# Kernel tuning notes

Hardware: AMD Instinct MI355X
Metric: run time of the kernel (lower is better)

The kernel has to match this reference:

```python
import jax, jax.numpy as jnp
import numpy as np

B, V, T, CIN, WEMB, H, NW = 32, 500, 24, 2, 4, 64, 8
C0 = CIN + WEMB  # 6 channels entering first layer


def _stglstm(x, supports, Wg, bg, Wo, bo, out_len=None, final_layer=False):
    # x: (B, C, V, T); supports: (S, V, V)
    Bb, C, Vv, Tt = x.shape
    T_steps = out_len if out_len is not None else Tt
    if final_layer:
        xs = jnp.broadcast_to(x[:, :, :, -1][None], (T_steps, Bb, C, Vv))
    else:
        xs = jnp.moveaxis(x, 3, 0)  # (T, B, C, V)

    def step(carry, xt):
        hx, cx = carry
        comb = xt + hx  # (B, C, V)
        feats = [comb]
        for s in range(supports.shape[0]):  # fixed small support_len loop
            x1 = jnp.einsum('bcv,vw->bcw', comb, supports[s])
            x2 = jnp.einsum('bcv,vw->bcw', x1, supports[s])
            feats += [x1, x2]  # order-2 diffusion
        g = jnp.concatenate(feats, axis=1)  # (B, 7C, V)
        gates = jnp.einsum('bgv,og->bov', g, Wg) + bg[None, :, None]  # (B, 4C, V)
        i, f, cg, o = jnp.split(gates, 4, axis=1)
        cy = jax.nn.sigmoid(f) * cx + jax.nn.sigmoid(i) * cg  # cellgate is linear (no tanh), as in source
        hy = jax.nn.sigmoid(o) * jnp.tanh(cy)
        return (hy, cy), hy

    h0 = jnp.zeros((Bb, C, Vv), x.dtype)
    _, hs = jax.lax.scan(step, (h0, h0), xs)  # hs: (T, B, C, V)
    hs = jnp.moveaxis(hs, 0, 3)  # (B, C, V, T)
    return jnp.einsum('bcvt,oc->bovt', hs, Wo) + bo[None, :, None, None]


def _se(x, Wa, Wb):
    y = x.mean(axis=(2, 3))  # (B, C) global avg pool
    y = jax.nn.sigmoid(jax.nn.relu(y @ Wa.T) @ Wb.T)
    return x * y[:, :, None, None]


def setup_inputs():
    key = jax.random.key(0)
    ks = jax.random.split(key, 24)

    def n(k, shape, s=0.05):
        return jax.random.normal(k, shape, jnp.float32) * s

    A = jax.random.uniform(ks[0], (3, V, V), jnp.float32)
    A = A / A.sum(-1, keepdims=True)  # row-stochastic random-walk matrices
    return {
        'x': n(ks[1], (B, CIN, V, T), 1.0),
        'supports': A,
        'w_type': jax.random.randint(ks[2], (B, V, T), 0, NW, dtype=jnp.int32),
        'Wemb': n(ks[3], (NW, WEMB)),
        'Wg0': n(ks[4], (4 * C0, 7 * C0)), 'bg0': jnp.zeros((4 * C0,), jnp.float32),
        'Wo0': n(ks[5], (H, C0)), 'bo0': jnp.zeros((H,), jnp.float32),
        'Ws0a': n(ks[6], (H // 16, H)), 'Ws0b': n(ks[7], (H, H // 16)),
        'Wg1': n(ks[8], (4 * H, 7 * H)), 'bg1': jnp.zeros((4 * H,), jnp.float32),
        'Wo1': n(ks[9], (H, H)), 'bo1': jnp.zeros((H,), jnp.float32),
        'Ws1a': n(ks[10], (H // 16, H)), 'Ws1b': n(ks[11], (H, H // 16)),
        'Wg2': n(ks[12], (4 * H, 7 * H)), 'bg2': jnp.zeros((4 * H,), jnp.float32),
        'Wo2': n(ks[13], (H, H)), 'bo2': jnp.zeros((H,), jnp.float32),
        'Wg3': n(ks[14], (4 * H, 7 * H)), 'bg3': jnp.zeros((4 * H,), jnp.float32),
        'Wo3': n(ks[15], (2, H)), 'bo3': jnp.zeros((2,), jnp.float32),
    }


def reference(x, supports, w_type, Wemb, Wg0, bg0, Wo0, bo0, Ws0a, Ws0b,
              Wg1, bg1, Wo1, bo1, Ws1a, Ws1b, Wg2, bg2, Wo2, bo2,
              Wg3, bg3, Wo3, bo3):
    w_vec = Wemb[w_type]  # (B, V, T, wemb)
    w_vec = jnp.transpose(w_vec, (0, 3, 1, 2))  # (B, wemb, V, T)
    h = jnp.concatenate([x, w_vec], axis=1)  # (B, CIN+wemb, V, T)
    h = _stglstm(h, supports, Wg0, bg0, Wo0, bo0)
    h = _se(h, Ws0a, Ws0b)
    h = _stglstm(h, supports, Wg1, bg1, Wo1, bo1)
    h = _se(h, Ws1a, Ws1b)
    h = _stglstm(h, supports, Wg2, bg2, Wo2, bo2)
    out = _stglstm(h, supports, Wg3, bg3, Wo3, bo3, out_len=T, final_layer=True)
    return out  # (B, 2, V, out_len)
```

## Files before the change

kernel.cpp:

```cpp
#include <hip/hip_runtime.h>
#include <math.h>

#define NV 500
#define NB 32
#define NT 24
#define NH 64

typedef _Float16 f16;
typedef _Float16 f16x8 __attribute__((ext_vector_type(8)));
typedef _Float16 f16x4 __attribute__((ext_vector_type(4)));
typedef float    f32x4 __attribute__((ext_vector_type(4)));

__device__ __forceinline__ float sigm(float x){ return 1.f/(1.f+expf(-x)); }

__global__ void k_a2(const float* __restrict__ A, float* __restrict__ A2)
{
    int idx = blockIdx.x*256 + threadIdx.x;
    if (idx >= 3*500*500) return;
    int wv = idx % 500; int rest = idx/500; int r = rest % 500; int s = rest/500;
    const float* Ar = A + ((size_t)s*500 + r)*500;
    const float* Ac = A + (size_t)s*500*500 + wv;
    float a = 0.f;
    for (int u = 0; u < 500; u++) a += Ar[u]*Ac[(size_t)u*500];
    A2[idx] = a;
}

__global__ void k_acat(const float* __restrict__ A, const float* __restrict__ A2,
                       f16* __restrict__ AcatT)
{
    int idx = blockIdx.x*256 + threadIdx.x;
    if (idx >= 3072*512) return;
    int k = idx & 511;
    int n = idx >> 9;
    int j = n >> 9, wv = n & 511;
    float val = 0.f;
    if (k < 500 && wv < 500) {
        int s = j >> 1;
        const float* M = (j & 1) ? A2 : A;
        val = M[((size_t)s*500 + k)*500 + wv];
    }
    AcatT[idx] = (f16)val;
}

__global__ void k_f2h(const float* __restrict__ src, f16* __restrict__ dst, int n)
{
    int idx = blockIdx.x*256 + threadIdx.x;
    if (idx < n) dst[idx] = (f16)src[idx];
}

__global__ __launch_bounds__(256)
void k_diff(const f16* __restrict__ Acv, const f16* __restrict__ Bt,
            f16* __restrict__ fout, int Mtot, int C, int G)
{
    __shared__ f16 lA[128*32];
    __shared__ f16 lB[128*32];
    const int tid = threadIdx.x;
    const int n0 = blockIdx.x*128, m0 = blockIdx.y*128;
    const int r0 = tid>>2, c0 = tid&3;
    const int swz0 = r0*32 + ((c0 ^ ((r0>>1)&3))<<3);
    const int swz1 = swz0 + 64*32;
    int mA0 = m0 + r0;      if (mA0 > Mtot-1) mA0 = Mtot-1;
    int mA1 = m0 + r0 + 64; if (mA1 > Mtot-1) mA1 = Mtot-1;
    const f16* gA0 = Acv + (size_t)mA0*512 + c0*8;
    const f16* gA1 = Acv + (size_t)mA1*512 + c0*8;
    const f16* gB0 = Bt + (size_t)(n0+r0)*512 + c0*8;
    const f16* gB1 = Bt + (size_t)(n0+r0+64)*512 + c0*8;

    const int w = tid>>6, lane = tid&63;
    const int wr = (w>>1)<<6, wc = (w&1)<<6;
    const int fm = lane&15, fk = lane>>4;
    const int fch = (fk ^ ((fm>>1)&3))<<3;

    f32x4 acc[4][4];
    #pragma unroll
    for (int i=0;i<4;i++)
        #pragma unroll
        for (int j=0;j<4;j++) acc[i][j] = (f32x4){0.f,0.f,0.f,0.f};

    f32x4 ra0 = *(const f32x4*)gA0, ra1 = *(const f32x4*)gA1;
    f32x4 rb0 = *(const f32x4*)gB0, rb1 = *(const f32x4*)gB1;

    for (int ks = 0; ks < 16; ks++) {
        __syncthreads();
        *(f32x4*)(lA + swz0) = ra0;  *(f32x4*)(lA + swz1) = ra1;
        *(f32x4*)(lB + swz0) = rb0;  *(f32x4*)(lB + swz1) = rb1;
        if (ks < 15) {
            int o = (ks+1)*32;
            ra0 = *(const f32x4*)(gA0 + o); ra1 = *(const f32x4*)(gA1 + o);
            rb0 = *(const f32x4*)(gB0 + o); rb1 = *(const f32x4*)(gB1 + o);
        }
        __syncthreads();
        f16x8 af[4], bf[4];
        #pragma unroll
        for (int i=0;i<4;i++) af[i] = *(const f16x8*)(lA + (wr + i*16 + fm)*32 + fch);
        #pragma unroll
        for (int j=0;j<4;j++) bf[j] = *(const f16x8*)(lB + (wc + j*16 + fm)*32 + fch);
        #pragma unroll
        for (int i=0;i<4;i++)
            #pragma unroll
            for (int j=0;j<4;j++)
                acc[i][j] = __builtin_amdgcn_mfma_f32_16x16x32_f16(af[i], bf[j], acc[i][j], 0, 0, 0);
    }

    #pragma unroll
    for (int j=0;j<4;j++) {
        int col = n0 + wc + j*16 + fm;
        int jb = col >> 9, wv = col & 511;
        if (wv >= 500) continue;
        #pragma unroll
        for (int i=0;i<4;i++) {
            int mb = m0 + wr + i*16 + fk*4;
            if (C == 64) {
                if (mb >= Mtot) continue;
                int b = mb >> 6, c = mb & 63;
                f16x4 h4;
                h4[0]=(f16)acc[i][j][0]; h4[1]=(f16)acc[i][j][1];
                h4[2]=(f16)acc[i][j][2]; h4[3]=(f16)acc[i][j][3];
                *(f16x4*)(fout + ((size_t)b*512 + wv)*G + C + jb*C + c) = h4;
            } else {
                #pragma unroll
                for (int r=0;r<4;r++) {
                    int m = mb + r;
                    if (m < Mtot) {
                        int b = m / C, c = m - b*C;
                        fout[((size_t)b*512 + wv)*G + C + jb*C + c] = (f16)acc[i][j][r];
                    }
                }
            }
        }
    }
}

__global__ __launch_bounds__(256)
void k_gates(const f16* __restrict__ fT, const f16* __restrict__ Wg,
             const float* __restrict__ bg, float* __restrict__ gT)
{
    __shared__ f16 lA[128*32];
    __shared__ f16 lB[128*32];
    const int tid = threadIdx.x;
    const int n0 = blockIdx.x*128, m0 = blockIdx.y*128, b = blockIdx.z;
    const f16* Ab = fT + (size_t)b*512*448;
    const int r0 = tid>>2, c0 = tid&3;
    const int swz0 = r0*32 + ((c0 ^ ((r0>>1)&3))<<3);
    const int swz1 = swz0 + 64*32;
    const f16* gA0 = Ab + (size_t)(m0+r0)*448 + c0*8;
    const f16* gA1 = Ab + (size_t)(m0+r0+64)*448 + c0*8;
    const f16* gB0 = Wg + (size_t)(n0+r0)*448 + c0*8;
    const f16* gB1 = Wg + (size_t)(n0+r0+64)*448 + c0*8;

    const int w = tid>>6, lane = tid&63;
    const int wr = (w>>1)<<6, wc = (w&1)<<6;
    const int fm = lane&15, fk = lane>>4;
    const int fch = (fk ^ ((fm>>1)&3))<<3;

    f32x4 acc[4][4];
    #pragma unroll
    for (int i=0;i<4;i++)
        #pragma unroll
        for (int j=0;j<4;j++) acc[i][j] = (f32x4){0.f,0.f,0.f,0.f};

    f32x4 ra0 = *(const f32x4*)gA0, ra1 = *(const f32x4*)gA1;
    f32x4 rb0 = *(const f32x4*)gB0, rb1 = *(const f32x4*)gB1;

    for (int ks = 0; ks < 14; ks++) {
        __syncthreads();
        *(f32x4*)(lA + swz0) = ra0;  *(f32x4*)(lA + swz1) = ra1;
        *(f32x4*)(lB + swz0) = rb0;  *(f32x4*)(lB + swz1) = rb1;
        if (ks < 13) {
            int o = (ks+1)*32;
            ra0 = *(const f32x4*)(gA0 + o); ra1 = *(const f32x4*)(gA1 + o);
            rb0 = *(const f32x4*)(gB0 + o); rb1 = *(const f32x4*)(gB1 + o);
        }
        __syncthreads();
        f16x8 af[4], bf[4];
        #pragma unroll
        for (int i=0;i<4;i++) af[i] = *(const f16x8*)(lA + (wr + i*16 + fm)*32 + fch);
        #pragma unroll
        for (int j=0;j<4;j++) bf[j] = *(const f16x8*)(lB + (wc + j*16 + fm)*32 + fch);
        #pragma unroll
        for (int i=0;i<4;i++)
            #pragma unroll
            for (int j=0;j<4;j++)
                acc[i][j] = __builtin_amdgcn_mfma_f32_16x16x32_f16(af[i], bf[j], acc[i][j], 0, 0, 0);
    }

    #pragma unroll
    for (int j=0;j<4;j++) {
        int o = n0 + wc + j*16 + fm;
        float bias = bg[o];
        #pragma unroll
        for (int i=0;i<4;i++) {
            int vb = m0 + wr + i*16 + fk*4;
            #pragma unroll
            for (int r=0;r<4;r++) {
                int v = vb + r;
                if (v < 500)
                    gT[((size_t)b*512 + v)*256 + o] = acc[i][j][r] + bias;
            }
        }
    }
}

__global__ __launch_bounds__(256)
void k_comb(const void* __restrict__ src, int srcF16, int Cin,
            const float* __restrict__ Wo, const float* __restrict__ bo,
            const float* __restrict__ se, const f16* __restrict__ hprev,
            f16* __restrict__ fT, f16* __restrict__ ccv)
{
    __shared__ float WoS[64*64];
    __shared__ float seS[64], boS[64];
    __shared__ f16 combS[64*72];
    int b = blockIdx.y, v0 = blockIdx.x*64;
    int tid = threadIdx.x;
    if (Cin > 0) {
        for (int i = tid; i < 64*Cin; i += 256) WoS[i] = Wo[i];
        if (tid < 64) { boS[tid] = bo[tid]; seS[tid] = se ? se[b*64+tid] : 1.f; }
    }
    __syncthreads();
    int vloc = tid>>2, part = tid&3;
    int v = v0 + vloc;
    float val[16];
    if (Cin == 0) {
        const float* x3 = (const float*)src + ((size_t)b*512 + v)*64 + part*16;
        #pragma unroll
        for (int k=0;k<16;k++) val[k] = x3[k];
    } else {
        float acc[16];
        #pragma unroll
        for (int k=0;k<16;k++) acc[k] = 0.f;
        if (srcF16) {
            const f16* sp = (const f16*)src + ((size_t)b*512 + v)*64;
            for (int cc=0; cc<Cin; cc++) {
                float xv = (float)sp[cc];
                #pragma unroll
                for (int k=0;k<16;k++) acc[k] += WoS[(part*16+k)*Cin + cc]*xv;
            }
        } else {
            const float* sp = (const float*)src + ((size_t)b*512 + v)*(size_t)Cin;
            for (int cc=0; cc<Cin; cc++) {
                float xv = sp[cc];
                #pragma unroll
                for (int k=0;k<16;k++) acc[k] += WoS[(part*16+k)*Cin + cc]*xv;
            }
        }
        #pragma unroll
        for (int k=0;k<16;k++) { int c = part*16+k; val[k] = seS[c]*(acc[k] + boS[c]); }
    }
    if (hprev) {
        const f16* hp = hprev + ((size_t)b*512 + v)*64 + part*16;
        #pragma unroll
        for (int k=0;k<16;k++) val[k] += (float)hp[k];
    }
    if (v >= 500) {
        #pragma unroll
        for (int k=0;k<16;k++) val[k] = 0.f;
    }
    #pragma unroll
    for (int k=0;k<16;k++) combS[vloc*72 + part*16 + k] = (f16)val[k];
    __syncthreads();
    {
        int vl = tid>>2, p = tid&3;
        f32x4 d0 = *(f32x4*)(combS + vl*72 + p*16);
        f32x4 d1 = *(f32x4*)(combS + vl*72 + p*16 + 8);
        f16* dst = fT + ((size_t)b*512 + (v0+vl))*448 + p*16;
        *(f32x4*)dst = d0; *(f32x4*)(dst+8) = d1;
    }
    {
        int c = tid>>2, p = tid&3;
        alignas(16) f16 tmp[16];
        #pragma unroll
        for (int k=0;k<16;k++) tmp[k] = combS[(p*16+k)*72 + c];
        f16* dst = ccv + ((size_t)b*64 + c)*512 + v0 + p*16;
        *(f32x4*)dst = *(f32x4*)tmp; *(f32x4*)(dst+8) = *(f32x4*)(tmp+8);
    }
}

__global__ void k_lstm(const float* __restrict__ gT, float* __restrict__ cst,
                       f16* __restrict__ hdst, int first)
{
    int id = blockIdx.x*4 + (threadIdx.x>>6);
    if (id >= NB*500) return;
    int b = id / 500, v = id - b*500;
    int c = threadIdx.x & 63;
    const float* g = gT + ((size_t)b*512 + v)*256;
    float gi = g[c], gf = g[64+c], gc = g[128+c], go = g[192+c];
    size_t ci = ((size_t)b*512 + v)*64 + c;
    float cx = first ? 0.f : cst[ci];
    float cy = sigm(gf)*cx + sigm(gi)*gc;
    cst[ci] = cy;
    hdst[ci] = (f16)(sigm(go)*tanhf(cy));
}

__global__ void k_lstm3out(const float* __restrict__ gT, float* __restrict__ cst,
                           f16* __restrict__ hdst, const float* __restrict__ Wo3,
                           const float* __restrict__ bo3, float* __restrict__ out,
                           int t, int first)
{
    int id = blockIdx.x*4 + (threadIdx.x>>6);
    if (id >= NB*500) return;
    int b = id / 500, v = id - b*500;
    int c = threadIdx.x & 63;
    const float* g = gT + ((size_t)b*512 + v)*256;
    float gi = g[c], gf = g[64+c], gc = g[128+c], go = g[192+c];
    size_t ci = ((size_t)b*512 + v)*64 + c;
    float cx = first ? 0.f : cst[ci];
    float cy = sigm(gf)*cx + sigm(gi)*gc;
    cst[ci] = cy;
    float hy = sigm(go)*tanhf(cy);
    hdst[ci] = (f16)hy;
    float r0 = Wo3[c]*hy, r1 = Wo3[64+c]*hy;
    #pragma unroll
    for (int s = 32; s > 0; s >>= 1) {
        r0 += __shfl_down(r0, s, 64);
        r1 += __shfl_down(r1, s, 64);
    }
    if (c == 0) {
        out[((size_t)(b*2+0)*500 + v)*24 + t] = r0 + bo3[0];
        out[((size_t)(b*2+1)*500 + v)*24 + t] = r1 + bo3[1];
    }
}

__global__ void k_comb0(const float* __restrict__ x, const int* __restrict__ wt,
                        const float* __restrict__ Wemb, const float* __restrict__ hs0T,
                        f16* __restrict__ f0T, f16* __restrict__ ccv0, int t)
{
    int b = blockIdx.y;
    int v = blockIdx.x*256 + threadIdx.x;
    if (v >= 512) return;
    if (v >= 500) {
        #pragma unroll
        for (int c=0;c<6;c++) ccv0[((size_t)b*6 + c)*512 + v] = (f16)0.f;
        return;
    }
    float vals[6];
    vals[0] = x[((size_t)(b*2+0)*500 + v)*24 + t];
    vals[1] = x[((size_t)(b*2+1)*500 + v)*24 + t];
    int wty = wt[((size_t)b*500 + v)*24 + t];
    vals[2] = Wemb[wty*4+0]; vals[3] = Wemb[wty*4+1];
    vals[4] = Wemb[wty*4+2]; vals[5] = Wemb[wty*4+3];
    if (t > 0) {
        const float* hp = hs0T + (((size_t)(t-1)*NB + b)*512 + v)*6;
        #pragma unroll
        for (int c=0;c<6;c++) vals[c] += hp[c];
    }
    #pragma unroll
    for (int c=0;c<6;c++) {
        f16 h = (f16)vals[c];
        f0T[((size_t)b*512 + v)*42 + c] = h;
        ccv0[((size_t)b*6 + c)*512 + v] = h;
    }
}

__global__ void k_gates0(const float* __restrict__ Wg, const float* __restrict__ bgv,
                         const f16* __restrict__ f0T, float* __restrict__ g0T)
{
    __shared__ float WgS[24*42];
    for (int i = threadIdx.x; i < 24*42; i += 256) WgS[i] = Wg[i];
    __syncthreads();
    int idx = blockIdx.x*256 + threadIdx.x;
    if (idx >= NB*24*500) return;
    int v = idx % 500; int rest = idx/500; int o = rest % 24; int b = rest/24;
    const f16* fp = f0T + ((size_t)b*512 + v)*42;
    float a = bgv[o];
    #pragma unroll
    for (int g = 0; g < 42; g++) a += WgS[o*42+g]*(float)fp[g];
    g0T[((size_t)b*512 + v)*24 + o] = a;
}

__global__ void k_lstm0(const float* __restrict__ g0T, float* __restrict__ cst0,
                        float* __restrict__ hs0T, int t)
{
    int idx = blockIdx.x*256 + threadIdx.x;
    if (idx >= NB*500*6) return;
    int c = idx % 6; int rest = idx/6; int v = rest % 500; int b = rest/500;
    const float* g = g0T + ((size_t)b*512 + v)*24;
    float gi = g[c], gf = g[6+c], gc = g[12+c], go = g[18+c];
    size_t ci = ((size_t)b*500 + v)*6 + c;
    float cx = t ? cst0[ci] : 0.f;
    float cy = sigm(gf)*cx + sigm(gi)*gc;
    cst0[ci] = cy;
    hs0T[(((size_t)t*NB + b)*512 + v)*6 + c] = sigm(go)*tanhf(cy);
}

__global__ void k_mean0(const float* __restrict__ hs0T, float* __restrict__ mean0)
{
    int b = blockIdx.x;
    float acc[6] = {0,0,0,0,0,0};
    for (int i = threadIdx.x; i < 24*500; i += 256) {
        int tt = i/500, v = i - tt*500;
        const float* p = hs0T + (((size_t)tt*NB + b)*512 + v)*6;
        #pragma unroll
        for (int c=0;c<6;c++) acc[c] += p[c];
    }
    __shared__ float red[256];
    for (int c=0;c<6;c++) {
        red[threadIdx.x] = acc[c]; __syncthreads();
        for (int s=128;s>0;s>>=1) { if (threadIdx.x<s) red[threadIdx.x]+=red[threadIdx.x+s]; __syncthreads(); }
        if (threadIdx.x==0) mean0[b*6+c] = red[0]/12000.f;
        __syncthreads();
    }
}

__global__ void k_mean1(const f16* __restrict__ hs1T, float* __restrict__ mean1)
{
    int cg = blockIdx.x, b = blockIdx.y;
    float acc[8] = {0,0,0,0,0,0,0,0};
    for (int i = threadIdx.x; i < 24*500; i += 256) {
        int tt = i/500, v = i - tt*500;
        const f16* p = hs1T + (((size_t)tt*NB + b)*512 + v)*64 + cg*8;
        #pragma unroll
        for (int c=0;c<8;c++) acc[c] += (float)p[c];
    }
    __shared__ float red[256];
    for (int c=0;c<8;c++) {
        red[threadIdx.x] = acc[c]; __syncthreads();
        for (int s=128;s>0;s>>=1) { if (threadIdx.x<s) red[threadIdx.x]+=red[threadIdx.x+s]; __syncthreads(); }
        if (threadIdx.x==0) mean1[b*64 + cg*8 + c] = red[0]/12000.f;
        __syncthreads();
    }
}

__global__ void k_se(const float* __restrict__ meanhs, const float* __restrict__ Wo,
                     const float* __restrict__ bo, int Cin,
                     const float* __restrict__ Wa, const float* __restrict__ Wb,
                     float* __restrict__ se)
{
    int b = blockIdx.x; int c = threadIdx.x;
    __shared__ float y[64]; __shared__ float a[4];
    float acc = bo[c];
    for (int j = 0; j < Cin; j++) acc += Wo[(size_t)c*Cin + j] * meanhs[b*Cin + j];
    y[c] = acc;
    __syncthreads();
    if (c < 4) {
        float s = 0.f;
        for (int j = 0; j < 64; j++) s += Wa[c*64 + j] * y[j];
        a[c] = fmaxf(s, 0.f);
    }
    __syncthreads();
    float s = 0.f;
    #pragma unroll
    for (int j = 0; j < 4; j++) s += Wb[c*4 + j] * a[j];
    se[b*64 + c] = 1.f/(1.f + expf(-s));
}

__global__ void k_x3(const f16* __restrict__ h, const float* __restrict__ Wo,
                     const float* __restrict__ bo, float* __restrict__ x3T)
{
    int idx = blockIdx.x*256 + threadIdx.x;
    if (idx >= NB*500*64) return;
    int c = idx & 63; int rest = idx >> 6; int v = rest % 500; int b = rest/500;
    const f16* hp = h + ((size_t)b*512 + v)*64;
    float a = bo[c];
    #pragma unroll 8
    for (int cc = 0; cc < 64; cc++) a += Wo[c*64 + cc]*(float)hp[cc];
    x3T[((size_t)b*512 + v)*64 + c] = a;
}

extern "C" void kernel_launch(void* const* d_in, const int* in_sizes, int n_in,
                              void* d_out, int out_size, void* d_ws, size_t ws_size,
                              hipStream_t stream)
{
    const float* x    = (const float*)d_in[0];
    const float* sup  = (const float*)d_in[1];
    const int*   wt   = (const int*)  d_in[2];
    const float* Wemb = (const float*)d_in[3];
    const float* Wg0  = (const float*)d_in[4];
    const float* bg0  = (const float*)d_in[5];
    const float* Wo0  = (const float*)d_in[6];
    const float* bo0  = (const float*)d_in[7];
    const float* Wa0  = (const float*)d_in[8];
    const float* Wb0  = (const float*)d_in[9];
    const float* Wg1  = (const float*)d_in[10];
    const float* bg1  = (const float*)d_in[11];
    const float* Wo1  = (const float*)d_in[12];
    const float* bo1  = (const float*)d_in[13];
    const float* Wa1  = (const float*)d_in[14];
    const float* Wb1  = (const float*)d_in[15];
    const float* Wg2  = (const float*)d_in[16];
    const float* bg2  = (const float*)d_in[17];
    const float* Wo2  = (const float*)d_in[18];
    const float* bo2  = (const float*)d_in[19];
    const float* Wg3  = (const float*)d_in[20];
    const float* bg3  = (const float*)d_in[21];
    const float* Wo3  = (const float*)d_in[22];
    const float* bo3  = (const float*)d_in[23];
    float* out = (float*)d_out;
    (void)in_sizes; (void)n_in; (void)out_size; (void)ws_size;

    char* ws = (char*)d_ws;
    size_t off = 0;
    f16*   AcatT  = (f16*)(ws + off);   off += (size_t)3072*512*2;
    float* A2     = (float*)(ws + off); off += (size_t)3*500*500*4;
    f16*   WgF1   = (f16*)(ws + off);   off += (size_t)256*448*2;
    f16*   WgF2   = (f16*)(ws + off);   off += (size_t)256*448*2;
    f16*   WgF3   = (f16*)(ws + off);   off += (size_t)256*448*2;
    f16*   comb_cv= (f16*)(ws + off);   off += (size_t)2048*512*2;
    f16*   ccv0   = (f16*)(ws + off);   off += (size_t)192*512*2;
    f16*   featsT = (f16*)(ws + off);   off += (size_t)NB*512*448*2;
    f16*   f0T    = (f16*)(ws + off);   off += (size_t)NB*512*42*2;
    float* gatesT = (float*)(ws + off); off += (size_t)NB*512*256*4;
    float* g0T    = (float*)(ws + off); off += (size_t)NB*512*24*4;
    float* hs0T   = (float*)(ws + off); off += (size_t)NT*NB*512*6*4;
    f16*   hs1T   = (f16*)(ws + off);   off += (size_t)NT*NB*512*64*2;
    f16*   hT     = (f16*)(ws + off);   off += (size_t)NB*512*64*2;
    float* cstT   = (float*)(ws + off); off += (size_t)NB*512*64*4;
    float* cst0   = (float*)(ws + off); off += (size_t)NB*500*6*4;
    float* x3T    = (float*)(ws + off); off += (size_t)NB*512*64*4;
    float* mean0  = (float*)(ws + off); off += 8192;
    float* se0    = (float*)(ws + off); off += 8192;
    float* mean1  = (float*)(ws + off); off += 8192;
    float* se1    = (float*)(ws + off); off += 8192;

    const size_t sliceH = (size_t)NB*512*64;
    const size_t slice0 = (size_t)NB*512*6;

    k_a2  <<<(3*500*500 + 255)/256, 256, 0, stream>>>(sup, A2);
    k_acat<<<(3072*512 + 255)/256, 256, 0, stream>>>(sup, A2, AcatT);
    k_f2h <<<(256*448 + 255)/256, 256, 0, stream>>>(Wg1, WgF1, 256*448);
    k_f2h <<<(256*448 + 255)/256, 256, 0, stream>>>(Wg2, WgF2, 256*448);
    k_f2h <<<(256*448 + 255)/256, 256, 0, stream>>>(Wg3, WgF3, 256*448);

    for (int t = 0; t < NT; t++) {
        k_comb0 <<<dim3(2, NB), 256, 0, stream>>>(x, wt, Wemb, hs0T, f0T, ccv0, t);
        k_diff  <<<dim3(24, 2), 256, 0, stream>>>(ccv0, AcatT, f0T, 192, 6, 42);
        k_gates0<<<(NB*24*500 + 255)/256, 256, 0, stream>>>(Wg0, bg0, f0T, g0T);
        k_lstm0 <<<(NB*500*6 + 255)/256, 256, 0, stream>>>(g0T, cst0, hs0T, t);
    }
    k_mean0<<<NB, 256, 0, stream>>>(hs0T, mean0);
    k_se   <<<NB, 64, 0, stream>>>(mean0, Wo0, bo0, 6, Wa0, Wb0, se0);

    for (int t = 0; t < NT; t++) {
        k_comb <<<dim3(8, NB), 256, 0, stream>>>(hs0T + (size_t)t*slice0, 0, 6,
                 Wo0, bo0, se0, t ? hs1T + (size_t)(t-1)*sliceH : (const f16*)nullptr,
                 featsT, comb_cv);
        k_diff <<<dim3(24, 16), 256, 0, stream>>>(comb_cv, AcatT, featsT, 2048, 64, 448);
        k_gates<<<dim3(2, 4, NB), 256, 0, stream>>>(featsT, WgF1, bg1, gatesT);
        k_lstm <<<4000, 256, 0, stream>>>(gatesT, cstT, hs1T + (size_t)t*sliceH, t == 0);
    }
    k_mean1<<<dim3(8, NB), 256, 0, stream>>>(hs1T, mean1);
    k_se   <<<NB, 64, 0, stream>>>(mean1, Wo1, bo1, 64, Wa1, Wb1, se1);

    for (int t = 0; t < NT; t++) {
        k_comb <<<dim3(8, NB), 256, 0, stream>>>(hs1T + (size_t)t*sliceH, 1, 64,
                 Wo1, bo1, se1, t ? hT : (const f16*)nullptr, featsT, comb_cv);
        k_diff <<<dim3(24, 16), 256, 0, stream>>>(comb_cv, AcatT, featsT, 2048, 64, 448);
        k_gates<<<dim3(2, 4, NB), 256, 0, stream>>>(featsT, WgF2, bg2, gatesT);
        k_lstm <<<4000, 256, 0, stream>>>(gatesT, cstT, hT, t == 0);
    }
    k_x3<<<(NB*500*64 + 255)/256, 256, 0, stream>>>(hT, Wo2, bo2, x3T);

    for (int t = 0; t < NT; t++) {
        k_comb <<<dim3(8, NB), 256, 0, stream>>>(x3T, 0, 0,
                 (const float*)nullptr, (const float*)nullptr, (const float*)nullptr,
                 t ? hT : (const f16*)nullptr, featsT, comb_cv);
        k_diff <<<dim3(24, 16), 256, 0, stream>>>(comb_cv, AcatT, featsT, 2048, 64, 448);
        k_gates<<<dim3(2, 4, NB), 256, 0, stream>>>(featsT, WgF3, bg3, gatesT);
        k_lstm3out<<<4000, 256, 0, stream>>>(gatesT, cstT, hT, Wo3, bo3, out, t, t == 0);
    }
}
```

Baseline: 4.362 ms.

## Fuse layer-0 gates/LSTM, MFMA A^2 precompute, fp16 gate buffer, padded Wo smem

```diff
diff --git a/kernel.cpp b/kernel.cpp
--- a/kernel.cpp
+++ b/kernel.cpp
@@ -13,33 +13,95 @@
 
 __device__ __forceinline__ float sigm(float x){ return 1.f/(1.f+expf(-x)); }
 
-__global__ void k_a2(const float* __restrict__ A, float* __restrict__ A2)
-{
-    int idx = blockIdx.x*256 + threadIdx.x;
-    if (idx >= 3*500*500) return;
-    int wv = idx % 500; int rest = idx/500; int r = rest % 500; int s = rest/500;
-    const float* Ar = A + ((size_t)s*500 + r)*500;
-    const float* Ac = A + (size_t)s*500*500 + wv;
-    float a = 0.f;
-    for (int u = 0; u < 500; u++) a += Ar[u]*Ac[(size_t)u*500];
-    A2[idx] = a;
-}
-
-__global__ void k_acat(const float* __restrict__ A, const float* __restrict__ A2,
-                       f16* __restrict__ AcatT)
-{
-    int idx = blockIdx.x*256 + threadIdx.x;
-    if (idx >= 3072*512) return;
-    int k = idx & 511;
-    int n = idx >> 9;
-    int j = n >> 9, wv = n & 511;
-    float val = 0.f;
-    if (k < 500 && wv < 500) {
-        int s = j >> 1;
-        const float* M = (j & 1) ? A2 : A;
-        val = M[((size_t)s*500 + k)*500 + wv];
-    }
-    AcatT[idx] = (f16)val;
+__global__ __launch_bounds__(256)
+void k_prep_a(const float* __restrict__ A, f16* __restrict__ AcatT, f16* __restrict__ A16)
+{
+    __shared__ float t[64][65];
+    const int s = blockIdx.z;
+    const int v0 = blockIdx.y*64, w0 = blockIdx.x*64;
+    const float* As = A + (size_t)s*500*500;
+    const int tid = threadIdx.x;
+    for (int e = tid; e < 64*64; e += 256) {
+        int r = e>>6, c = e&63;
+        int v = v0+r, w = w0+c;
+        float val = (v < 500 && w < 500) ? As[(size_t)v*500 + w] : 0.f;
+        t[r][c] = val;
+        A16[((size_t)s*512 + v)*512 + w] = (f16)val;
+    }
+    __syncthreads();
+    for (int e = tid; e < 64*64; e += 256) {
+        int wr = e>>6, vc = e&63;
+        AcatT[((size_t)(2*s)*512 + w0+wr)*512 + v0+vc] = (f16)t[vc][wr];
+    }
+}
+
+__global__ __launch_bounds__(256)
+void k_a2m(f16* __restrict__ AcatT, const f16* __restrict__ A16)
+{
+    __shared__ f16 lA[128*32];
+    __shared__ f16 lB[128*32];
+    const int tid = threadIdx.x;
+    const int s = blockIdx.z;
+    const int n0 = blockIdx.x*128, m0 = blockIdx.y*128;
+    const f16* AT = AcatT + (size_t)(2*s)*512*512;
+    const f16* Y  = A16 + (size_t)s*512*512;
+    f16* D = AcatT + (size_t)(2*s+1)*512*512;
+
+    const int r0 = tid>>2, c0 = tid&3;
+    const int swz0 = r0*32 + ((c0 ^ ((r0>>1)&3))<<3);
+    const int swz1 = swz0 + 64*32;
+    const f16* gA0 = AT + (size_t)(m0+r0)*512 + c0*8;
+    const f16* gA1 = AT + (size_t)(m0+r0+64)*512 + c0*8;
+    const f16* gB0 = Y + (size_t)(n0+r0)*512 + c0*8;
+    const f16* gB1 = Y + (size_t)(n0+r0+64)*512 + c0*8;
+
+    const int w = tid>>6, lane = tid&63;
+    const int wr = (w>>1)<<6, wc = (w&1)<<6;
+    const int fm = lane&15, fk = lane>>4;
+    const int fch = (fk ^ ((fm>>1)&3))<<3;
+
+    f32x4 acc[4][4];
+    #pragma unroll
+    for (int i=0;i<4;i++)
+        #pragma unroll
+        for (int j=0;j<4;j++) acc[i][j] = (f32x4){0.f,0.f,0.f,0.f};
+
+    f32x4 ra0 = *(const f32x4*)gA0, ra1 = *(const f32x4*)gA1;
+    f32x4 rb0 = *(const f32x4*)gB0, rb1 = *(const f32x4*)gB1;
+
+    for (int ks = 0; ks < 16; ks++) {
+        __syncthreads();
+        *(f32x4*)(lA + swz0) = ra0;  *(f32x4*)(lA + swz1) = ra1;
+        *(f32x4*)(lB + swz0) = rb0;  *(f32x4*)(lB + swz1) = rb1;
+        if (ks < 15) {
+            int o = (ks+1)*32;
+            ra0 = *(const f32x4*)(gA0 + o); ra1 = *(const f32x4*)(gA1 + o);
+            rb0 = *(const f32x4*)(gB0 + o); rb1 = *(const f32x4*)(gB1 + o);
+        }
+        __syncthreads();
+        f16x8 af[4], bf[4];
+        #pragma unroll
+        for (int i=0;i<4;i++) af[i] = *(const f16x8*)(lA + (wr + i*16 + fm)*32 + fch);
+        #pragma unroll
+        for (int j=0;j<4;j++) bf[j] = *(const f16x8*)(lB + (wc + j*16 + fm)*32 + fch);
+        #pragma unroll
+        for (int i=0;i<4;i++)
+            #pragma unroll
+            for (int j=0;j<4;j++)
+                acc[i][j] = __builtin_amdgcn_mfma_f32_16x16x32_f16(af[i], bf[j], acc[i][j], 0, 0, 0);
+    }
+
+    #pragma unroll
+    for (int j=0;j<4;j++) {
+        int col = n0 + wc + j*16 + fm;
+        #pragma unroll
+        for (int i=0;i<4;i++) {
+            int mb = m0 + wr + i*16 + fk*4;
+            #pragma unroll
+            for (int r=0;r<4;r++)
+                D[(size_t)(mb+r)*512 + col] = (f16)acc[i][j][r];
+        }
+    }
 }
 
 __global__ void k_f2h(const float* __restrict__ src, f16* __restrict__ dst, int n)
@@ -133,7 +195,7 @@
 
 __global__ __launch_bounds__(256)
 void k_gates(const f16* __restrict__ fT, const f16* __restrict__ Wg,
-             const float* __restrict__ bg, float* __restrict__ gT)
+             const float* __restrict__ bg, f16* __restrict__ gT)
 {
     __shared__ f16 lA[128*32];
     __shared__ f16 lB[128*32];
@@ -195,7 +257,7 @@
             for (int r=0;r<4;r++) {
                 int v = vb + r;
                 if (v < 500)
-                    gT[((size_t)b*512 + v)*256 + o] = acc[i][j][r] + bias;
+                    gT[((size_t)b*512 + v)*256 + o] = (f16)(acc[i][j][r] + bias);
             }
         }
     }
@@ -207,13 +269,17 @@
             const float* __restrict__ se, const f16* __restrict__ hprev,
             f16* __restrict__ fT, f16* __restrict__ ccv)
 {
-    __shared__ float WoS[64*64];
+    __shared__ float WoS[64*65];
     __shared__ float seS[64], boS[64];
     __shared__ f16 combS[64*72];
     int b = blockIdx.y, v0 = blockIdx.x*64;
     int tid = threadIdx.x;
+    const int PS = Cin | 1;
     if (Cin > 0) {
-        for (int i = tid; i < 64*Cin; i += 256) WoS[i] = Wo[i];
+        for (int i = tid; i < 64*Cin; i += 256) {
+            int r = i / Cin, cc = i - r*Cin;
+            WoS[r*PS + cc] = Wo[i];
+        }
         if (tid < 64) { boS[tid] = bo[tid]; seS[tid] = se ? se[b*64+tid] : 1.f; }
     }
     __syncthreads();
@@ -233,14 +299,14 @@
             for (int cc=0; cc<Cin; cc++) {
                 float xv = (float)sp[cc];
                 #pragma unroll
-                for (int k=0;k<16;k++) acc[k] += WoS[(part*16+k)*Cin + cc]*xv;
+                for (int k=0;k<16;k++) acc[k] += WoS[(part*16+k)*PS + cc]*xv;
             }
         } else {
             const float* sp = (const float*)src + ((size_t)b*512 + v)*(size_t)Cin;
             for (int cc=0; cc<Cin; cc++) {
                 float xv = sp[cc];
                 #pragma unroll
-                for (int k=0;k<16;k++) acc[k] += WoS[(part*16+k)*Cin + cc]*xv;
+                for (int k=0;k<16;k++) acc[k] += WoS[(part*16+k)*PS + cc]*xv;
             }
         }
         #pragma unroll
@@ -275,15 +341,15 @@
     }
 }
 
-__global__ void k_lstm(const float* __restrict__ gT, float* __restrict__ cst,
+__global__ void k_lstm(const f16* __restrict__ gT, float* __restrict__ cst,
                        f16* __restrict__ hdst, int first)
 {
     int id = blockIdx.x*4 + (threadIdx.x>>6);
     if (id >= NB*500) return;
     int b = id / 500, v = id - b*500;
     int c = threadIdx.x & 63;
-    const float* g = gT + ((size_t)b*512 + v)*256;
-    float gi = g[c], gf = g[64+c], gc = g[128+c], go = g[192+c];
+    const f16* g = gT + ((size_t)b*512 + v)*256;
+    float gi = (float)g[c], gf = (float)g[64+c], gc = (float)g[128+c], go = (float)g[192+c];
     size_t ci = ((size_t)b*512 + v)*64 + c;
     float cx = first ? 0.f : cst[ci];
     float cy = sigm(gf)*cx + sigm(gi)*gc;
@@ -291,7 +357,7 @@
     hdst[ci] = (f16)(sigm(go)*tanhf(cy));
 }
 
-__global__ void k_lstm3out(const float* __restrict__ gT, float* __restrict__ cst,
+__global__ void k_lstm3out(const f16* __restrict__ gT, float* __restrict__ cst,
                            f16* __restrict__ hdst, const float* __restrict__ Wo3,
                            const float* __restrict__ bo3, float* __restrict__ out,
                            int t, int first)
@@ -300,8 +366,8 @@
     if (id >= NB*500) return;
     int b = id / 500, v = id - b*500;
     int c = threadIdx.x & 63;
-    const float* g = gT + ((size_t)b*512 + v)*256;
-    float gi = g[c], gf = g[64+c], gc = g[128+c], go = g[192+c];
+    const f16* g = gT + ((size_t)b*512 + v)*256;
+    float gi = (float)g[c], gf = (float)g[64+c], gc = (float)g[128+c], go = (float)g[192+c];
     size_t ci = ((size_t)b*512 + v)*64 + c;
     float cx = first ? 0.f : cst[ci];
     float cy = sigm(gf)*cx + sigm(gi)*gc;
@@ -320,66 +386,83 @@
     }
 }
 
-__global__ void k_comb0(const float* __restrict__ x, const int* __restrict__ wt,
-                        const float* __restrict__ Wemb, const float* __restrict__ hs0T,
-                        f16* __restrict__ f0T, f16* __restrict__ ccv0, int t)
-{
-    int b = blockIdx.y;
-    int v = blockIdx.x*256 + threadIdx.x;
-    if (v >= 512) return;
-    if (v >= 500) {
-        #pragma unroll
-        for (int c=0;c<6;c++) ccv0[((size_t)b*6 + c)*512 + v] = (f16)0.f;
-        return;
-    }
-    float vals[6];
-    vals[0] = x[((size_t)(b*2+0)*500 + v)*24 + t];
-    vals[1] = x[((size_t)(b*2+1)*500 + v)*24 + t];
-    int wty = wt[((size_t)b*500 + v)*24 + t];
-    vals[2] = Wemb[wty*4+0]; vals[3] = Wemb[wty*4+1];
-    vals[4] = Wemb[wty*4+2]; vals[5] = Wemb[wty*4+3];
-    if (t > 0) {
-        const float* hp = hs0T + (((size_t)(t-1)*NB + b)*512 + v)*6;
-        #pragma unroll
-        for (int c=0;c<6;c++) vals[c] += hp[c];
-    }
-    #pragma unroll
-    for (int c=0;c<6;c++) {
-        f16 h = (f16)vals[c];
-        f0T[((size_t)b*512 + v)*42 + c] = h;
+__global__ void k_xe(const float* __restrict__ x, const int* __restrict__ wt,
+                     const float* __restrict__ Wemb, float* __restrict__ XE)
+{
+    int id = blockIdx.x*256 + threadIdx.x;
+    if (id >= NT*NB*512) return;
+    int v = id & 511; int r = id >> 9; int b = r & 31; int t = r >> 5;
+    float vals[6] = {0.f,0.f,0.f,0.f,0.f,0.f};
+    if (v < 500) {
+        vals[0] = x[((size_t)(b*2+0)*500 + v)*24 + t];
+        vals[1] = x[((size_t)(b*2+1)*500 + v)*24 + t];
+        int wty = wt[((size_t)b*500 + v)*24 + t];
+        vals[2] = Wemb[wty*4+0]; vals[3] = Wemb[wty*4+1];
+        vals[4] = Wemb[wty*4+2]; vals[5] = Wemb[wty*4+3];
+    }
+    float* xe = XE + (size_t)id*6;
+    #pragma unroll
+    for (int c = 0; c < 6; c++) xe[c] = vals[c];
+}
+
+__global__ void k_seed0(const float* __restrict__ XE, f16* __restrict__ f0T,
+                        f16* __restrict__ ccv0)
+{
+    int id = blockIdx.x*256 + threadIdx.x;
+    if (id >= NB*512) return;
+    int v = id & 511, b = id >> 9;
+    const float* xe = XE + (size_t)id*6;
+    #pragma unroll
+    for (int c = 0; c < 6; c++) {
+        f16 h = (v < 500) ? (f16)xe[c] : (f16)0.f;
+        f0T[(size_t)id*42 + c] = h;
         ccv0[((size_t)b*6 + c)*512 + v] = h;
     }
 }
 
-__global__ void k_gates0(const float* __restrict__ Wg, const float* __restrict__ bgv,
-                         const f16* __restrict__ f0T, float* __restrict__ g0T)
+__global__ __launch_bounds__(256)
+void k_glstm0(f16* f0T, const float* __restrict__ Wg0,
+              const float* __restrict__ bg0, float* __restrict__ cst0,
+              float* __restrict__ hs0T, const float* __restrict__ XE,
+              f16* __restrict__ ccv0, int t)
 {
     __shared__ float WgS[24*42];
-    for (int i = threadIdx.x; i < 24*42; i += 256) WgS[i] = Wg[i];
+    __shared__ float bgS[24];
+    int tid = threadIdx.x;
+    for (int i = tid; i < 24*42; i += 256) WgS[i] = Wg0[i];
+    if (tid < 24) bgS[tid] = bg0[tid];
     __syncthreads();
-    int idx = blockIdx.x*256 + threadIdx.x;
-    if (idx >= NB*24*500) return;
-    int v = idx % 500; int rest = idx/500; int o = rest % 24; int b = rest/24;
+    int id = blockIdx.x*256 + tid;
+    if (id >= NB*500) return;
+    int b = id / 500, v = id - b*500;
     const f16* fp = f0T + ((size_t)b*512 + v)*42;
-    float a = bgv[o];
-    #pragma unroll
-    for (int g = 0; g < 42; g++) a += WgS[o*42+g]*(float)fp[g];
-    g0T[((size_t)b*512 + v)*24 + o] = a;
-}
-
-__global__ void k_lstm0(const float* __restrict__ g0T, float* __restrict__ cst0,
-                        float* __restrict__ hs0T, int t)
-{
-    int idx = blockIdx.x*256 + threadIdx.x;
-    if (idx >= NB*500*6) return;
-    int c = idx % 6; int rest = idx/6; int v = rest % 500; int b = rest/500;
-    const float* g = g0T + ((size_t)b*512 + v)*24;
-    float gi = g[c], gf = g[6+c], gc = g[12+c], go = g[18+c];
-    size_t ci = ((size_t)b*500 + v)*6 + c;
-    float cx = t ? cst0[ci] : 0.f;
-    float cy = sigm(gf)*cx + sigm(gi)*gc;
-    cst0[ci] = cy;
-    hs0T[(((size_t)t*NB + b)*512 + v)*6 + c] = sigm(go)*tanhf(cy);
+    float fv[42];
+    #pragma unroll
+    for (int g = 0; g < 42; g++) fv[g] = (float)fp[g];
+    float gates[24];
+    #pragma unroll
+    for (int o = 0; o < 24; o++) {
+        float a = bgS[o];
+        #pragma unroll
+        for (int g = 0; g < 42; g++) a += WgS[o*42+g]*fv[g];
+        gates[o] = a;
+    }
+    size_t hrow = (((size_t)t*NB + b)*512 + v)*6;
+    const float* xe = XE + (((size_t)(t+1)*NB + b)*512 + v)*6;
+    #pragma unroll
+    for (int c = 0; c < 6; c++) {
+        size_t ci = ((size_t)b*500 + v)*6 + c;
+        float cx = t ? cst0[ci] : 0.f;
+        float cy = sigm(gates[6+c])*cx + sigm(gates[c])*gates[12+c];
+        cst0[ci] = cy;
+        float h = sigm(gates[18+c])*tanhf(cy);
+        hs0T[hrow + c] = h;
+        if (t < 23) {
+            float cmb = xe[c] + h;
+            f0T[((size_t)b*512 + v)*42 + c] = (f16)cmb;
+            ccv0[((size_t)b*6 + c)*512 + v] = (f16)cmb;
+        }
+    }
 }
 
 __global__ void k_mean0(const float* __restrict__ hs0T, float* __restrict__ mean0)
@@ -490,7 +573,7 @@
     char* ws = (char*)d_ws;
     size_t off = 0;
     f16*   AcatT  = (f16*)(ws + off);   off += (size_t)3072*512*2;
-    float* A2     = (float*)(ws + off); off += (size_t)3*500*500*4;
+    f16*   A16    = (f16*)(ws + off);   off += (size_t)3*512*512*2;
     f16*   WgF1   = (f16*)(ws + off);   off += (size_t)256*448*2;
     f16*   WgF2   = (f16*)(ws + off);   off += (size_t)256*448*2;
     f16*   WgF3   = (f16*)(ws + off);   off += (size_t)256*448*2;
@@ -498,8 +581,8 @@
     f16*   ccv0   = (f16*)(ws + off);   off += (size_t)192*512*2;
     f16*   featsT = (f16*)(ws + off);   off += (size_t)NB*512*448*2;
     f16*   f0T    = (f16*)(ws + off);   off += (size_t)NB*512*42*2;
-    float* gatesT = (float*)(ws + off); off += (size_t)NB*512*256*4;
-    float* g0T    = (float*)(ws + off); off += (size_t)NB*512*24*4;
+    f16*   gatesT = (f16*)(ws + off);   off += (size_t)NB*512*256*2;
+    float* XE     = (float*)(ws + off); off += (size_t)NT*NB*512*6*4;
     float* hs0T   = (float*)(ws + off); off += (size_t)NT*NB*512*6*4;
     f16*   hs1T   = (f16*)(ws + off);   off += (size_t)NT*NB*512*64*2;
     f16*   hT     = (f16*)(ws + off);   off += (size_t)NB*512*64*2;
@@ -514,17 +597,17 @@
     const size_t sliceH = (size_t)NB*512*64;
     const size_t slice0 = (size_t)NB*512*6;
 
-    k_a2  <<<(3*500*500 + 255)/256, 256, 0, stream>>>(sup, A2);
-    k_acat<<<(3072*512 + 255)/256, 256, 0, stream>>>(sup, A2, AcatT);
+    k_prep_a<<<dim3(8, 8, 3), 256, 0, stream>>>(sup, AcatT, A16);
+    k_a2m   <<<dim3(4, 4, 3), 256, 0, stream>>>(AcatT, A16);
     k_f2h <<<(256*448 + 255)/256, 256, 0, stream>>>(Wg1, WgF1, 256*448);
     k_f2h <<<(256*448 + 255)/256, 256, 0, stream>>>(Wg2, WgF2, 256*448);
     k_f2h <<<(256*448 + 255)/256, 256, 0, stream>>>(Wg3, WgF3, 256*448);
-
+    k_xe  <<<(NT*NB*512)/256, 256, 0, stream>>>(x, wt, Wemb, XE);
+
+    k_seed0<<<(NB*512)/256, 256, 0, stream>>>(XE, f0T, ccv0);
     for (int t = 0; t < NT; t++) {
-        k_comb0 <<<dim3(2, NB), 256, 0, stream>>>(x, wt, Wemb, hs0T, f0T, ccv0, t);
         k_diff  <<<dim3(24, 2), 256, 0, stream>>>(ccv0, AcatT, f0T, 192, 6, 42);
-        k_gates0<<<(NB*24*500 + 255)/256, 256, 0, stream>>>(Wg0, bg0, f0T, g0T);
-        k_lstm0 <<<(NB*500*6 + 255)/256, 256, 0, stream>>>(g0T, cst0, hs0T, t);
+        k_glstm0<<<(NB*500 + 255)/256, 256, 0, stream>>>(f0T, Wg0, bg0, cst0, hs0T, XE, ccv0, t);
     }
     k_mean0<<<NB, 256, 0, stream>>>(hs0T, mean0);
     k_se   <<<NB, 64, 0, stream>>>(mean0, Wo0, bo0, 6, Wa0, Wb0, se0);
```

Result: slower. 5.368 ms (+23.1%).
